# Kernel tuning notes

Hardware: AMD Instinct MI355X
Metric: run time of the kernel (lower is better)

## Reference

```python
import jax, jax.numpy as jnp
import numpy as np

# HEAD_ORDER column indices: predictor=0, cf_perm=1, cf_primary=2, cf_secondary=3, reorder=4, interleave=5
# emb rows follow sorted(used_heads) = ['cf_perm','cf_primary','cf_secondary','predictor','reorder']
_HEAD_ROW = {'cf_perm': 0, 'cf_primary': 1, 'cf_secondary': 2, 'predictor': 3, 'reorder': 4}
_HEAD_COL = {'predictor': 0, 'cf_perm': 1, 'cf_primary': 2, 'cf_secondary': 3, 'reorder': 4, 'interleave': 5}
_PAIRS = [('predictor', 'cf_perm'), ('predictor', 'cf_primary'), ('predictor', 'cf_secondary'),
          ('reorder', 'cf_perm'), ('reorder', 'cf_primary'), ('reorder', 'cf_secondary')]
_SCALE = 1.0

BATCH, NEGS, INPUT_DIM, DIM, VOCAB, N_HEADS = 2048, 512, 256, 64, 32, 5


def setup_inputs() -> dict:
    key = jax.random.key(0)
    ks = jax.random.split(key, 5)
    x = jax.random.normal(ks[0], (BATCH, INPUT_DIM), dtype=jnp.float32)
    neg_labels = jax.random.randint(ks[1], (BATCH, NEGS, 6), 0, VOCAB, dtype=jnp.int64)
    emb = jax.random.normal(ks[2], (N_HEADS, VOCAB, DIM), dtype=jnp.float32)
    gate_w = jax.random.normal(ks[3], (6, DIM, INPUT_DIM), dtype=jnp.float32) * (INPUT_DIM ** -0.5)
    gate_b = jax.random.normal(ks[4], (6, DIM), dtype=jnp.float32) * 0.01
    return {'x': x, 'neg_labels': neg_labels, 'emb': emb, 'gate_w': gate_w, 'gate_b': gate_b}


def reference(x, neg_labels, emb, gate_w, gate_b):
    # gates for all 6 pairs at once: (6, batch, dim)
    g = jnp.tanh(jnp.einsum('bi,pdi->pbd', x, gate_w) + gate_b[:, None, :])
    score = jnp.zeros((neg_labels.shape[0], neg_labels.shape[1]), dtype=x.dtype)
    for p, (a, b) in enumerate(_PAIRS):
        ea = emb[_HEAD_ROW[a]][neg_labels[:, :, _HEAD_COL[a]]]  # (batch, negs, dim)
        eb = emb[_HEAD_ROW[b]][neg_labels[:, :, _HEAD_COL[b]]]  # (batch, negs, dim)
        score = score + jnp.einsum('bnd,bd,bnd->bn', ea, g[p], eb)
    return score * _SCALE
```

## Files before the change

### kernel.cpp

```cpp
#include <hip/hip_runtime.h>
#include <hip/hip_bf16.h>

typedef __bf16 bf16x8 __attribute__((ext_vector_type(8)));
typedef float f32x4 __attribute__((ext_vector_type(4)));

#define BATCH 2048
#define NEGS 512
#define IN_DIM 256
#define NGATE 384
#define EMB_LD 72
#define TAB_LD 34

__device__ inline bf16x8 cvt8(float4 f0, float4 f1) {
    bf16x8 r;
    r[0] = (__bf16)f0.x; r[1] = (__bf16)f0.y; r[2] = (__bf16)f0.z; r[3] = (__bf16)f0.w;
    r[4] = (__bf16)f1.x; r[5] = (__bf16)f1.y; r[6] = (__bf16)f1.z; r[7] = (__bf16)f1.w;
    return r;
}

__global__ __launch_bounds__(256) void gate_gemm_kernel(
    const float* __restrict__ x, const float* __restrict__ gw,
    const float* __restrict__ gb, __bf16* __restrict__ g)
{
    const int w = threadIdx.x >> 6, l = threadIdx.x & 63;
    const int lm = l & 15, lq = l >> 4;
    const int tile = blockIdx.x * 4 + w;
    const int mt = tile / 24, nt = tile % 24;
    const int m0 = mt * 16, n0 = nt * 16;

    const float* xp = x + (size_t)(m0 + lm) * IN_DIM + lq * 8;
    const float* wp = gw + (size_t)(n0 + lm) * IN_DIM + lq * 8;
    f32x4 acc = {};
#pragma unroll
    for (int s = 0; s < 8; ++s) {
        bf16x8 a = cvt8(*(const float4*)(xp + s * 32), *(const float4*)(xp + s * 32 + 4));
        bf16x8 b = cvt8(*(const float4*)(wp + s * 32), *(const float4*)(wp + s * 32 + 4));
        acc = __builtin_amdgcn_mfma_f32_16x16x32_bf16(a, b, acc, 0, 0, 0);
    }
    const int col = n0 + lm;
    const float bias = gb[col];
#pragma unroll
    for (int r = 0; r < 4; ++r) {
        const int row = m0 + lq * 4 + r;
        g[(size_t)row * NGATE + col] = (__bf16)tanhf(acc[r] + bias);
    }
}

__global__ __launch_bounds__(256, 3) void table_score_kernel(
    const int* __restrict__ labels, const float* __restrict__ emb,
    const __bf16* __restrict__ g, float* __restrict__ out)
{
    __shared__ __align__(16) __bf16 embs[5 * 32 * EMB_LD];
    __shared__ __align__(16) __bf16 tab[2 * 6 * 32 * TAB_LD];

    const int t = threadIdx.x;
    const int b0 = blockIdx.x * 2;
    const int w = t >> 6, l = t & 63;
    const int lm = l & 15, lq = l >> 4;

    int4 q[2][3];
#pragma unroll
    for (int bi = 0; bi < 2; ++bi) {
        const int4* lp = (const int4*)(labels + (size_t)(b0 + bi) * NEGS * 6) + 3 * t;
        q[bi][0] = lp[0]; q[bi][1] = lp[1]; q[bi][2] = lp[2];
    }
    bf16x8 gv[3][2];
#pragma unroll
    for (int j = 0; j < 3; ++j) {
        const int id = w + j * 4;
        const int bi = id / 6, p = id % 6;
        const __bf16* gp = g + (size_t)(b0 + bi) * NGATE + p * 64 + lq * 8;
        gv[j][0] = *(const bf16x8*)gp;
        gv[j][1] = *(const bf16x8*)(gp + 32);
    }

#pragma unroll
    for (int c = 0; c < 5; ++c) {
        const int j = t + c * 256;
        const int head = j >> 8;
        const int rem = j & 255;
        const int v = rem >> 3, qq = rem & 7;
        const float4* src = (const float4*)(emb + (size_t)j * 8);
        bf16x8 val = cvt8(src[0], src[1]);
        *(bf16x8*)&embs[head * (32 * EMB_LD) + v * EMB_LD + qq * 8] = val;
    }
    __syncthreads();

#pragma unroll
    for (int j = 0; j < 3; ++j) {
        const int id = w + j * 4;
        const int p = id % 6;
        const int arow = (p < 3) ? 3 : 4;
        const int crow = (p < 3) ? p : p - 3;
        f32x4 acc[2][2] = {};

#pragma unroll
        for (int s = 0; s < 2; ++s) {
            const int k0 = s * 32 + lq * 8;
            float gf[8];
#pragma unroll
            for (int i = 0; i < 8; ++i) gf[i] = (float)gv[j][s][i];

            bf16x8 bfr[2], afr[2];
#pragma unroll
            for (int nh = 0; nh < 2; ++nh)
                bfr[nh] = *(const bf16x8*)&embs[crow * (32 * EMB_LD) + (nh * 16 + lm) * EMB_LD + k0];
#pragma unroll
            for (int mh = 0; mh < 2; ++mh) {
                bf16x8 ea = *(const bf16x8*)&embs[arow * (32 * EMB_LD) + (mh * 16 + lm) * EMB_LD + k0];
                bf16x8 r;
#pragma unroll
                for (int i = 0; i < 8; ++i) r[i] = (__bf16)((float)ea[i] * gf[i]);
                afr[mh] = r;
            }
#pragma unroll
            for (int mh = 0; mh < 2; ++mh)
#pragma unroll
                for (int nh = 0; nh < 2; ++nh)
                    acc[mh][nh] = __builtin_amdgcn_mfma_f32_16x16x32_bf16(afr[mh], bfr[nh], acc[mh][nh], 0, 0, 0);
        }

        __bf16* tb = tab + id * (32 * TAB_LD);
#pragma unroll
        for (int mh = 0; mh < 2; ++mh)
#pragma unroll
            for (int nh = 0; nh < 2; ++nh) {
                const int col = nh * 16 + lm;
#pragma unroll
                for (int r = 0; r < 4; ++r)
                    tb[(mh * 16 + lq * 4 + r) * TAB_LD + col] = (__bf16)acc[mh][nh][r];
            }
    }
    __syncthreads();

#pragma unroll
    for (int bi = 0; bi < 2; ++bi) {
        const int b = b0 + bi;
        const int4 q0 = q[bi][0];
        const int4 q1 = q[bi][1];
        const int4 q2 = q[bi][2];
        const __bf16* tb = tab + bi * (6 * 32 * TAB_LD);

        const float sA =
            (float)tb[0 * 32 * TAB_LD + q0.x * TAB_LD + q0.y] +
            (float)tb[1 * 32 * TAB_LD + q0.x * TAB_LD + q0.z] +
            (float)tb[2 * 32 * TAB_LD + q0.x * TAB_LD + q0.w] +
            (float)tb[3 * 32 * TAB_LD + q1.x * TAB_LD + q0.y] +
            (float)tb[4 * 32 * TAB_LD + q1.x * TAB_LD + q0.z] +
            (float)tb[5 * 32 * TAB_LD + q1.x * TAB_LD + q0.w];
        const float sB =
            (float)tb[0 * 32 * TAB_LD + q1.z * TAB_LD + q1.w] +
            (float)tb[1 * 32 * TAB_LD + q1.z * TAB_LD + q2.x] +
            (float)tb[2 * 32 * TAB_LD + q1.z * TAB_LD + q2.y] +
            (float)tb[3 * 32 * TAB_LD + q2.z * TAB_LD + q1.w] +
            (float)tb[4 * 32 * TAB_LD + q2.z * TAB_LD + q2.x] +
            (float)tb[5 * 32 * TAB_LD + q2.z * TAB_LD + q2.y];

        float2 res; res.x = sA; res.y = sB;
        *(float2*)(out + (size_t)b * NEGS + 2 * t) = res;
    }
}

extern "C" void kernel_launch(void* const* d_in, const int* in_sizes, int n_in,
                              void* d_out, int out_size, void* d_ws, size_t ws_size,
                              hipStream_t stream) {
    const float* x      = (const float*)d_in[0];
    const int*   labels = (const int*)d_in[1];
    const float* emb    = (const float*)d_in[2];
    const float* gw     = (const float*)d_in[3];
    const float* gb     = (const float*)d_in[4];
    float* out = (float*)d_out;
    __bf16* g  = (__bf16*)d_ws;

    hipLaunchKernelGGL(gate_gemm_kernel, dim3(768), dim3(256), 0, stream, x, gw, gb, g);
    hipLaunchKernelGGL(table_score_kernel, dim3(BATCH / 2), dim3(256), 0, stream,
                       labels, emb, g, out);
}
```

Measured before the change: 27.12 us.

## Process one batch row per block in table-score kernel and retune padding

Result: slower. 28.23 us (+4.1%).

```diff
diff --git a/kernel.cpp b/kernel.cpp
--- a/kernel.cpp
+++ b/kernel.cpp
@@ -9,7 +9,7 @@
 #define IN_DIM 256
 #define NGATE 384
 #define EMB_LD 72
-#define TAB_LD 34
+#define TAB_LD 33
 
 __device__ inline bf16x8 cvt8(float4 f0, float4 f1) {
     bf16x8 r;
@@ -18,7 +18,7 @@
     return r;
 }
 
-__global__ __launch_bounds__(256) void gate_gemm_kernel(
+__global__ __launch_bounds__(256, 4) void gate_gemm_kernel(
     const float* __restrict__ x, const float* __restrict__ gw,
     const float* __restrict__ gb, __bf16* __restrict__ g)
 {
@@ -31,7 +31,7 @@
     const float* xp = x + (size_t)(m0 + lm) * IN_DIM + lq * 8;
     const float* wp = gw + (size_t)(n0 + lm) * IN_DIM + lq * 8;
     f32x4 acc = {};
-#pragma unroll
+#pragma unroll 2
     for (int s = 0; s < 8; ++s) {
         bf16x8 a = cvt8(*(const float4*)(xp + s * 32), *(const float4*)(xp + s * 32 + 4));
         bf16x8 b = cvt8(*(const float4*)(wp + s * 32), *(const float4*)(wp + s * 32 + 4));
@@ -46,33 +46,22 @@
     }
 }
 
-__global__ __launch_bounds__(256, 3) void table_score_kernel(
+__global__ __launch_bounds__(256, 4) void table_score_kernel(
     const int* __restrict__ labels, const float* __restrict__ emb,
     const __bf16* __restrict__ g, float* __restrict__ out)
 {
     __shared__ __align__(16) __bf16 embs[5 * 32 * EMB_LD];
-    __shared__ __align__(16) __bf16 tab[2 * 6 * 32 * TAB_LD];
+    __shared__ __align__(16) __bf16 tab[6 * 32 * TAB_LD];
 
     const int t = threadIdx.x;
-    const int b0 = blockIdx.x * 2;
+    const int b = blockIdx.x;
     const int w = t >> 6, l = t & 63;
     const int lm = l & 15, lq = l >> 4;
 
-    int4 q[2][3];
-#pragma unroll
-    for (int bi = 0; bi < 2; ++bi) {
-        const int4* lp = (const int4*)(labels + (size_t)(b0 + bi) * NEGS * 6) + 3 * t;
-        q[bi][0] = lp[0]; q[bi][1] = lp[1]; q[bi][2] = lp[2];
-    }
-    bf16x8 gv[3][2];
-#pragma unroll
-    for (int j = 0; j < 3; ++j) {
-        const int id = w + j * 4;
-        const int bi = id / 6, p = id % 6;
-        const __bf16* gp = g + (size_t)(b0 + bi) * NGATE + p * 64 + lq * 8;
-        gv[j][0] = *(const bf16x8*)gp;
-        gv[j][1] = *(const bf16x8*)(gp + 32);
-    }
+    const int4* lp = (const int4*)(labels + (size_t)b * NEGS * 6) + 3 * t;
+    const int4 q0 = lp[0];
+    const int4 q1 = lp[1];
+    const int4 q2 = lp[2];
 
 #pragma unroll
     for (int c = 0; c < 5; ++c) {
@@ -86,20 +75,23 @@
     }
     __syncthreads();
 
-#pragma unroll
-    for (int j = 0; j < 3; ++j) {
-        const int id = w + j * 4;
-        const int p = id % 6;
+    for (int id = w; id < 6; id += 4) {
+        const int p = id;
         const int arow = (p < 3) ? 3 : 4;
         const int crow = (p < 3) ? p : p - 3;
+
+        const __bf16* gp = g + (size_t)b * NGATE + p * 64 + lq * 8;
+        const bf16x8 gva = *(const bf16x8*)gp;
+        const bf16x8 gvb = *(const bf16x8*)(gp + 32);
         f32x4 acc[2][2] = {};
 
 #pragma unroll
         for (int s = 0; s < 2; ++s) {
             const int k0 = s * 32 + lq * 8;
+            const bf16x8 gs = s ? gvb : gva;
             float gf[8];
 #pragma unroll
-            for (int i = 0; i < 8; ++i) gf[i] = (float)gv[j][s][i];
+            for (int i = 0; i < 8; ++i) gf[i] = (float)gs[i];
 
             bf16x8 bfr[2], afr[2];
 #pragma unroll
@@ -133,32 +125,23 @@
     }
     __syncthreads();
 
-#pragma unroll
-    for (int bi = 0; bi < 2; ++bi) {
-        const int b = b0 + bi;
-        const int4 q0 = q[bi][0];
-        const int4 q1 = q[bi][1];
-        const int4 q2 = q[bi][2];
-        const __bf16* tb = tab + bi * (6 * 32 * TAB_LD);
+    const float sA =
+        (float)tab[0 * 32 * TAB_LD + q0.x * TAB_LD + q0.y] +
+        (float)tab[1 * 32 * TAB_LD + q0.x * TAB_LD + q0.z] +
+        (float)tab[2 * 32 * TAB_LD + q0.x * TAB_LD + q0.w] +
+        (float)tab[3 * 32 * TAB_LD + q1.x * TAB_LD + q0.y] +
+        (float)tab[4 * 32 * TAB_LD + q1.x * TAB_LD + q0.z] +
+        (float)tab[5 * 32 * TAB_LD + q1.x * TAB_LD + q0.w];
+    const float sB =
+        (float)tab[0 * 32 * TAB_LD + q1.z * TAB_LD + q1.w] +
+        (float)tab[1 * 32 * TAB_LD + q1.z * TAB_LD + q2.x] +
+        (float)tab[2 * 32 * TAB_LD + q1.z * TAB_LD + q2.y] +
+        (float)tab[3 * 32 * TAB_LD + q2.z * TAB_LD + q1.w] +
+        (float)tab[4 * 32 * TAB_LD + q2.z * TAB_LD + q2.x] +
+        (float)tab[5 * 32 * TAB_LD + q2.z * TAB_LD + q2.y];
 
-        const float sA =
-            (float)tb[0 * 32 * TAB_LD + q0.x * TAB_LD + q0.y] +
-            (float)tb[1 * 32 * TAB_LD + q0.x * TAB_LD + q0.z] +
-            (float)tb[2 * 32 * TAB_LD + q0.x * TAB_LD + q0.w] +
-            (float)tb[3 * 32 * TAB_LD + q1.x * TAB_LD + q0.y] +
-            (float)tb[4 * 32 * TAB_LD + q1.x * TAB_LD + q0.z] +
-            (float)tb[5 * 32 * TAB_LD + q1.x * TAB_LD + q0.w];
-        const float sB =
-            (float)tb[0 * 32 * TAB_LD + q1.z * TAB_LD + q1.w] +
-            (float)tb[1 * 32 * TAB_LD + q1.z * TAB_LD + q2.x] +
-            (float)tb[2 * 32 * TAB_LD + q1.z * TAB_LD + q2.y] +
-            (float)tb[3 * 32 * TAB_LD + q2.z * TAB_LD + q1.w] +
-            (float)tb[4 * 32 * TAB_LD + q2.z * TAB_LD + q2.x] +
-            (float)tb[5 * 32 * TAB_LD + q2.z * TAB_LD + q2.y];
-
-        float2 res; res.x = sA; res.y = sB;
-        *(float2*)(out + (size_t)b * NEGS + 2 * t) = res;
-    }
+    float2 res; res.x = sA; res.y = sB;
+    *(float2*)(out + (size_t)b * NEGS + 2 * t) = res;
 }
 
 extern "C" void kernel_launch(void* const* d_in, const int* in_sizes, int n_in,
@@ -173,6 +156,6 @@
     __bf16* g  = (__bf16*)d_ws;
 
     hipLaunchKernelGGL(gate_gemm_kernel, dim3(768), dim3(256), 0, stream, x, gw, gb, g);
-    hipLaunchKernelGGL(table_score_kernel, dim3(BATCH / 2), dim3(256), 0, stream,
+    hipLaunchKernelGGL(table_score_kernel, dim3(BATCH), dim3(256), 0, stream,
                        labels, emb, g, out);
 }
```

## Fuse gate GEMM into pairwise table-score kernel with 8-row batch blocks

Applied to the files above, without the earlier changes.

New measurement: 30.45 us. 12.3% more time.

```diff
diff --git a/kernel.cpp b/kernel.cpp
--- a/kernel.cpp
+++ b/kernel.cpp
@@ -9,7 +9,7 @@
 #define IN_DIM 256
 #define NGATE 384
 #define EMB_LD 72
-#define TAB_LD 34
+#define TAB_LD 33
 
 __device__ inline bf16x8 cvt8(float4 f0, float4 f1) {
     bf16x8 r;
@@ -18,146 +18,159 @@
     return r;
 }
 
-__global__ __launch_bounds__(256) void gate_gemm_kernel(
-    const float* __restrict__ x, const float* __restrict__ gw,
-    const float* __restrict__ gb, __bf16* __restrict__ g)
-{
-    const int w = threadIdx.x >> 6, l = threadIdx.x & 63;
-    const int lm = l & 15, lq = l >> 4;
-    const int tile = blockIdx.x * 4 + w;
-    const int mt = tile / 24, nt = tile % 24;
-    const int m0 = mt * 16, n0 = nt * 16;
-
-    const float* xp = x + (size_t)(m0 + lm) * IN_DIM + lq * 8;
-    const float* wp = gw + (size_t)(n0 + lm) * IN_DIM + lq * 8;
-    f32x4 acc = {};
-#pragma unroll
-    for (int s = 0; s < 8; ++s) {
-        bf16x8 a = cvt8(*(const float4*)(xp + s * 32), *(const float4*)(xp + s * 32 + 4));
-        bf16x8 b = cvt8(*(const float4*)(wp + s * 32), *(const float4*)(wp + s * 32 + 4));
-        acc = __builtin_amdgcn_mfma_f32_16x16x32_bf16(a, b, acc, 0, 0, 0);
-    }
-    const int col = n0 + lm;
-    const float bias = gb[col];
-#pragma unroll
-    for (int r = 0; r < 4; ++r) {
-        const int row = m0 + lq * 4 + r;
-        g[(size_t)row * NGATE + col] = (__bf16)tanhf(acc[r] + bias);
-    }
-}
-
-__global__ __launch_bounds__(256, 3) void table_score_kernel(
-    const int* __restrict__ labels, const float* __restrict__ emb,
-    const __bf16* __restrict__ g, float* __restrict__ out)
+__global__ __launch_bounds__(512, 2) void fused_pairwise_kernel(
+    const float* __restrict__ x, const int* __restrict__ labels,
+    const float* __restrict__ emb, const float* __restrict__ gw,
+    const float* __restrict__ gb, float* __restrict__ out)
 {
     __shared__ __align__(16) __bf16 embs[5 * 32 * EMB_LD];
-    __shared__ __align__(16) __bf16 tab[2 * 6 * 32 * TAB_LD];
+    __shared__ __align__(16) __bf16 gls[8 * NGATE];
+    __shared__ __align__(16) __bf16 tab[24 * 32 * TAB_LD];
 
     const int t = threadIdx.x;
-    const int b0 = blockIdx.x * 2;
     const int w = t >> 6, l = t & 63;
     const int lm = l & 15, lq = l >> 4;
+    const int b0 = blockIdx.x * 8;
 
-    int4 q[2][3];
+    int4 lab[2][6];
 #pragma unroll
-    for (int bi = 0; bi < 2; ++bi) {
-        const int4* lp = (const int4*)(labels + (size_t)(b0 + bi) * NEGS * 6) + 3 * t;
-        q[bi][0] = lp[0]; q[bi][1] = lp[1]; q[bi][2] = lp[2];
-    }
-    bf16x8 gv[3][2];
+    for (int c = 0; c < 2; ++c) {
+        const int bb = b0 + c * 4 + (t >> 7);
+        const int4* lp = (const int4*)(labels + (size_t)bb * NEGS * 6 + (size_t)(t & 127) * 24);
 #pragma unroll
-    for (int j = 0; j < 3; ++j) {
-        const int id = w + j * 4;
-        const int bi = id / 6, p = id % 6;
-        const __bf16* gp = g + (size_t)(b0 + bi) * NGATE + p * 64 + lq * 8;
-        gv[j][0] = *(const bf16x8*)gp;
-        gv[j][1] = *(const bf16x8*)(gp + 32);
+        for (int i = 0; i < 6; ++i) lab[c][i] = lp[i];
     }
 
 #pragma unroll
-    for (int c = 0; c < 5; ++c) {
-        const int j = t + c * 256;
-        const int head = j >> 8;
-        const int rem = j & 255;
-        const int v = rem >> 3, qq = rem & 7;
-        const float4* src = (const float4*)(emb + (size_t)j * 8);
-        bf16x8 val = cvt8(src[0], src[1]);
-        *(bf16x8*)&embs[head * (32 * EMB_LD) + v * EMB_LD + qq * 8] = val;
+    for (int c = 0; c < 3; ++c) {
+        const int j = t + c * 512;
+        if (j < 1280) {
+            const int head = j >> 8, rem = j & 255;
+            const int v = rem >> 3, qq = rem & 7;
+            const float4* src = (const float4*)(emb + (size_t)j * 8);
+            *(bf16x8*)&embs[head * (32 * EMB_LD) + v * EMB_LD + qq * 8] = cvt8(src[0], src[1]);
+        }
+    }
+
+    {
+        const float* xp = x + (size_t)(b0 + (lm & 7)) * IN_DIM + lq * 8;
+        f32x4 acc[3] = {};
+#pragma unroll
+        for (int s = 0; s < 8; ++s) {
+            const bf16x8 a = cvt8(*(const float4*)(xp + s * 32), *(const float4*)(xp + s * 32 + 4));
+#pragma unroll
+            for (int j = 0; j < 3; ++j) {
+                const int nt = w * 3 + j;
+                const float* wp = gw + (size_t)(nt * 16 + lm) * IN_DIM + s * 32 + lq * 8;
+                const bf16x8 bv = cvt8(*(const float4*)wp, *(const float4*)(wp + 4));
+                acc[j] = __builtin_amdgcn_mfma_f32_16x16x32_bf16(a, bv, acc[j], 0, 0, 0);
+            }
+        }
+#pragma unroll
+        for (int j = 0; j < 3; ++j) {
+            const int col = (w * 3 + j) * 16 + lm;
+            const float bias = gb[col];
+#pragma unroll
+            for (int r = 0; r < 4; ++r) {
+                const int row = lq * 4 + r;
+                if (row < 8) gls[row * NGATE + col] = (__bf16)tanhf(acc[j][r] + bias);
+            }
+        }
     }
     __syncthreads();
 
-#pragma unroll
-    for (int j = 0; j < 3; ++j) {
-        const int id = w + j * 4;
-        const int p = id % 6;
-        const int arow = (p < 3) ? 3 : 4;
-        const int crow = (p < 3) ? p : p - 3;
-        f32x4 acc[2][2] = {};
+    for (int c = 0; c < 2; ++c) {
+        if (c) __syncthreads();
 
 #pragma unroll
-        for (int s = 0; s < 2; ++s) {
-            const int k0 = s * 32 + lq * 8;
-            float gf[8];
+        for (int j = 0; j < 3; ++j) {
+            const int id = w * 3 + j;
+            const int bi = id / 6, p = id % 6;
+            const int brow = c * 4 + bi;
+            const int arow = (p < 3) ? 3 : 4;
+            const int crow = (p < 3) ? p : p - 3;
+            f32x4 acc[2][2] = {};
+
 #pragma unroll
-            for (int i = 0; i < 8; ++i) gf[i] = (float)gv[j][s][i];
+            for (int s = 0; s < 2; ++s) {
+                const int k0 = s * 32 + lq * 8;
+                const bf16x8 gsv = *(const bf16x8*)(gls + brow * NGATE + p * 64 + k0);
+                float gf[8];
+#pragma unroll
+                for (int i = 0; i < 8; ++i) gf[i] = (float)gsv[i];
 
-            bf16x8 bfr[2], afr[2];
+                bf16x8 bfr[2], afr[2];
 #pragma unroll
-            for (int nh = 0; nh < 2; ++nh)
-                bfr[nh] = *(const bf16x8*)&embs[crow * (32 * EMB_LD) + (nh * 16 + lm) * EMB_LD + k0];
+                for (int nh = 0; nh < 2; ++nh)
+                    bfr[nh] = *(const bf16x8*)&embs[crow * (32 * EMB_LD) + (nh * 16 + lm) * EMB_LD + k0];
 #pragma unroll
-            for (int mh = 0; mh < 2; ++mh) {
-                bf16x8 ea = *(const bf16x8*)&embs[arow * (32 * EMB_LD) + (mh * 16 + lm) * EMB_LD + k0];
-                bf16x8 r;
+                for (int mh = 0; mh < 2; ++mh) {
+                    const bf16x8 ea = *(const bf16x8*)&embs[arow * (32 * EMB_LD) + (mh * 16 + lm) * EMB_LD + k0];
+                    bf16x8 r;
 #pragma unroll
-                for (int i = 0; i < 8; ++i) r[i] = (__bf16)((float)ea[i] * gf[i]);
-                afr[mh] = r;
+                    for (int i = 0; i < 8; ++i) r[i] = (__bf16)((float)ea[i] * gf[i]);
+                    afr[mh] = r;
+                }
+#pragma unroll
+                for (int mh = 0; mh < 2; ++mh)
+#pragma unroll
+                    for (int nh = 0; nh < 2; ++nh)
+                        acc[mh][nh] = __builtin_amdgcn_mfma_f32_16x16x32_bf16(afr[mh], bfr[nh], acc[mh][nh], 0, 0, 0);
             }
+
+            __bf16* tb = tab + id * (32 * TAB_LD);
 #pragma unroll
             for (int mh = 0; mh < 2; ++mh)
 #pragma unroll
-                for (int nh = 0; nh < 2; ++nh)
-                    acc[mh][nh] = __builtin_amdgcn_mfma_f32_16x16x32_bf16(afr[mh], bfr[nh], acc[mh][nh], 0, 0, 0);
+                for (int nh = 0; nh < 2; ++nh) {
+                    const int col = nh * 16 + lm;
+#pragma unroll
+                    for (int r = 0; r < 4; ++r)
+                        tb[(mh * 16 + lq * 4 + r) * TAB_LD + col] = (__bf16)acc[mh][nh][r];
+                }
         }
+        __syncthreads();
 
-        __bf16* tb = tab + id * (32 * TAB_LD);
-#pragma unroll
-        for (int mh = 0; mh < 2; ++mh)
-#pragma unroll
-            for (int nh = 0; nh < 2; ++nh) {
-                const int col = nh * 16 + lm;
-#pragma unroll
-                for (int r = 0; r < 4; ++r)
-                    tb[(mh * 16 + lq * 4 + r) * TAB_LD + col] = (__bf16)acc[mh][nh][r];
-            }
-    }
-    __syncthreads();
+        const int bi = t >> 7;
+        const __bf16* tb = tab + bi * (6 * 32 * TAB_LD);
+        const int4 l0 = lab[c][0], l1 = lab[c][1], l2 = lab[c][2];
+        const int4 l3 = lab[c][3], l4 = lab[c][4], l5 = lab[c][5];
 
-#pragma unroll
-    for (int bi = 0; bi < 2; ++bi) {
-        const int b = b0 + bi;
-        const int4 q0 = q[bi][0];
-        const int4 q1 = q[bi][1];
-        const int4 q2 = q[bi][2];
-        const __bf16* tb = tab + bi * (6 * 32 * TAB_LD);
-
-        const float sA =
-            (float)tb[0 * 32 * TAB_LD + q0.x * TAB_LD + q0.y] +
-            (float)tb[1 * 32 * TAB_LD + q0.x * TAB_LD + q0.z] +
-            (float)tb[2 * 32 * TAB_LD + q0.x * TAB_LD + q0.w] +
-            (float)tb[3 * 32 * TAB_LD + q1.x * TAB_LD + q0.y] +
-            (float)tb[4 * 32 * TAB_LD + q1.x * TAB_LD + q0.z] +
-            (float)tb[5 * 32 * TAB_LD + q1.x * TAB_LD + q0.w];
-        const float sB =
-            (float)tb[0 * 32 * TAB_LD + q1.z * TAB_LD + q1.w] +
-            (float)tb[1 * 32 * TAB_LD + q1.z * TAB_LD + q2.x] +
-            (float)tb[2 * 32 * TAB_LD + q1.z * TAB_LD + q2.y] +
-            (float)tb[3 * 32 * TAB_LD + q2.z * TAB_LD + q1.w] +
-            (float)tb[4 * 32 * TAB_LD + q2.z * TAB_LD + q2.x] +
-            (float)tb[5 * 32 * TAB_LD + q2.z * TAB_LD + q2.y];
-
-        float2 res; res.x = sA; res.y = sB;
-        *(float2*)(out + (size_t)b * NEGS + 2 * t) = res;
+        float4 res;
+        {
+            res.x = (float)tb[0 * 32 * TAB_LD + l0.x * TAB_LD + l0.y] +
+                    (float)tb[1 * 32 * TAB_LD + l0.x * TAB_LD + l0.z] +
+                    (float)tb[2 * 32 * TAB_LD + l0.x * TAB_LD + l0.w] +
+                    (float)tb[3 * 32 * TAB_LD + l1.x * TAB_LD + l0.y] +
+                    (float)tb[4 * 32 * TAB_LD + l1.x * TAB_LD + l0.z] +
+                    (float)tb[5 * 32 * TAB_LD + l1.x * TAB_LD + l0.w];
+        }
+        {
+            res.y = (float)tb[0 * 32 * TAB_LD + l1.z * TAB_LD + l1.w] +
+                    (float)tb[1 * 32 * TAB_LD + l1.z * TAB_LD + l2.x] +
+                    (float)tb[2 * 32 * TAB_LD + l1.z * TAB_LD + l2.y] +
+                    (float)tb[3 * 32 * TAB_LD + l2.z * TAB_LD + l1.w] +
+                    (float)tb[4 * 32 * TAB_LD + l2.z * TAB_LD + l2.x] +
+                    (float)tb[5 * 32 * TAB_LD + l2.z * TAB_LD + l2.y];
+        }
+        {
+            res.z = (float)tb[0 * 32 * TAB_LD + l3.x * TAB_LD + l3.y] +
+                    (float)tb[1 * 32 * TAB_LD + l3.x * TAB_LD + l3.z] +
+                    (float)tb[2 * 32 * TAB_LD + l3.x * TAB_LD + l3.w] +
+                    (float)tb[3 * 32 * TAB_LD + l4.x * TAB_LD + l3.y] +
+                    (float)tb[4 * 32 * TAB_LD + l4.x * TAB_LD + l3.z] +
+                    (float)tb[5 * 32 * TAB_LD + l4.x * TAB_LD + l3.w];
+        }
+        {
+            res.w = (float)tb[0 * 32 * TAB_LD + l4.z * TAB_LD + l4.w] +
+                    (float)tb[1 * 32 * TAB_LD + l4.z * TAB_LD + l5.x] +
+                    (float)tb[2 * 32 * TAB_LD + l4.z * TAB_LD + l5.y] +
+                    (float)tb[3 * 32 * TAB_LD + l5.z * TAB_LD + l4.w] +
+                    (float)tb[4 * 32 * TAB_LD + l5.z * TAB_LD + l5.x] +
+                    (float)tb[5 * 32 * TAB_LD + l5.z * TAB_LD + l5.y];
+        }
+        const int bb = b0 + c * 4 + bi;
+        *(float4*)(out + (size_t)bb * NEGS + (size_t)(t & 127) * 4) = res;
     }
 }
 
@@ -170,9 +183,7 @@
     const float* gw     = (const float*)d_in[3];
     const float* gb     = (const float*)d_in[4];
     float* out = (float*)d_out;
-    __bf16* g  = (__bf16*)d_ws;
 
-    hipLaunchKernelGGL(gate_gemm_kernel, dim3(768), dim3(256), 0, stream, x, gw, gb, g);
-    hipLaunchKernelGGL(table_score_kernel, dim3(BATCH / 2), dim3(256), 0, stream,
-                       labels, emb, g, out);
+    hipLaunchKernelGGL(fused_pairwise_kernel, dim3(BATCH / 8), dim3(512), 0, stream,
+                       x, labels, emb, gw, gb, out);
 }
```
